# Kernel tuning notes

Hardware: AMD Instinct MI355X
Metric: run time of the kernel (lower is better)

## Reference

```python
import jax, jax.numpy as jnp
import numpy as np

B = 64          # batch of trees
L = 10          # gated internal levels below the root
H = 256         # hidden_size
E = 256         # embed_size
V = 64          # embedding vocab (relation/role types)
TOTAL = 2 ** (L + 1) - 2   # heap layout: level i (1..L) has 2^i nodes at offset 2^i - 2


def setup_inputs() -> dict:
    key = jax.random.key(0)
    k = jax.random.split(key, 7)
    s = 0.05
    return {
        "node_ids": jax.random.randint(k[0], (B, TOTAL), 0, V, dtype=jnp.int32),
        "emb_table": jax.random.normal(k[1], (V, E), jnp.float32) * s,
        # W: x-projections, order (forget, input, output, update)
        "W": jax.random.normal(k[2], (4, E, H), jnp.float32) * s,
        "bW": jax.random.normal(k[3], (4, H), jnp.float32) * s,
        # U: hidden projections, [gate, child] with gate order
        # (forget_left, forget_right, input, output, update), child order (left, right)
        "U": jax.random.normal(k[4], (5, 2, H, H), jnp.float32) * s,
        "Ws": jax.random.normal(k[5], (2 * H, 3), jnp.float32) * s,
        "bs": jax.random.normal(k[6], (3,), jnp.float32) * s,
    }


def _tree_lstm(node_ids, emb_table, W, bW, U, Ws, bs):
    Bn, total = node_ids.shape
    Lv = int(np.log2(total + 2)) - 1          # number of gated levels (static)
    Hh = U.shape[-1]
    # Wforget is shared by both forget gates (as in the original module)
    gate_map = jnp.array([0, 0, 1, 2, 3])      # x-projection index per gate
    h = c = None
    for lev in range(Lv, 0, -1):               # leaves-up level order
        n = 2 ** lev
        off = 2 ** lev - 2
        ids = node_ids[:, off:off + n]         # [B, n]
        x = emb_table[ids]                     # [B, n, E]
        xg = jnp.einsum('bne,geh->gbnh', x, W) + bW[:, None, None, :]  # [4,B,n,H]
        if h is None:
            # deepest level: children are leaves -> zero h and c (init_hidden())
            hl = hr = cl = cr = jnp.zeros((Bn, n, Hh), x.dtype)
        else:
            hl, hr = h[:, 0::2], h[:, 1::2]
            cl, cr = c[:, 0::2], c[:, 1::2]
        pre = (jnp.einsum('bnh,ghk->gbnk', hl, U[:, 0])
               + jnp.einsum('bnh,ghk->gbnk', hr, U[:, 1])
               + xg[gate_map])                 # [5,B,n,H]
        f_l = jax.nn.sigmoid(pre[0])
        f_r = jax.nn.sigmoid(pre[1])
        i_g = jax.nn.sigmoid(pre[2])
        o_g = jax.nn.sigmoid(pre[3])
        u_g = jnp.tanh(pre[4])
        c = i_g * u_g + f_l * cl + f_r * cr
        h = o_g * jnp.tanh(c)
    # root: concatenate the two children's hidden states, then score
    root_hidden = jnp.concatenate([h[:, 0], h[:, 1]], axis=-1)   # [B, 2H]
    scores = root_hidden @ Ws + bs                               # [B, 3]
    return scores, root_hidden


def reference(node_ids, emb_table, W, bW, U, Ws, bs):
    return _tree_lstm(node_ids, emb_table, W, bW, U, Ws, bs)
```

## Files before the change

### kernel.cpp

```cpp
#include <hip/hip_runtime.h>
#include <hip/hip_bf16.h>
#include <stdint.h>
#include <math.h>


typedef __bf16 bf16x8 __attribute__((ext_vector_type(8)));
typedef float  f32x4  __attribute__((ext_vector_type(4)));
typedef int    i32x4  __attribute__((ext_vector_type(4)));

__device__ __forceinline__ float sigf(float x) { return 1.f / (1.f + __expf(-x)); }
__device__ __forceinline__ float tanhfast(float x) {
    return 1.f - 2.f / (__expf(2.f * x) + 1.f);
}

__global__ void prep_kernel(const float* __restrict__ emb, const float* __restrict__ W,
                            const float* __restrict__ bW, const float* __restrict__ U,
                            float* __restrict__ xg4, __bf16* __restrict__ BtP) {
    if (blockIdx.x < 256) {
        int g = blockIdx.x >> 6, v = blockIdx.x & 63, k = threadIdx.x;
        __shared__ float e[256];
        e[k] = emb[v * 256 + k];
        __syncthreads();
        float s = bW[g * 256 + k];
        const float* Wg = W + g * 65536 + k;
#pragma unroll 4
        for (int i = 0; i < 256; i++) s += e[i] * Wg[i * 256];
        xg4[(v * 256 + k) * 4 + g] = s;
    } else {
        int t = (blockIdx.x - 256) * 256 + threadIdx.x;
        int g    = t >> 14;
        int r    = t & 16383;
        int ct   = r >> 10;
        int ks   = (r >> 6) & 15;
        int lane = t & 63;
        int lr = lane & 15, q = lane >> 4;
        int col = ct * 16 + lr;
        int kbase = ks * 32 + q * 8;
        bf16x8 v8;
#pragma unroll
        for (int e2 = 0; e2 < 8; e2++) {
            int k = kbase + e2;
            int s = k >> 8, kk = k & 255;
            v8[e2] = (__bf16)U[((g * 2 + s) * 256 + kk) * 256 + col];
        }
        *(bf16x8*)(BtP + (long)t * 8) = v8;
    }
}

__global__ void leaf_kernel(const int* __restrict__ ids, const float* __restrict__ xg4,
                            __bf16* __restrict__ h, __bf16* __restrict__ c) {
    int col = threadIdx.x;
    int r0 = blockIdx.x * 32;
    for (int r = r0; r < r0 + 32; r++) {
        int b = r >> 10, j = r & 1023;
        int id = ids[b * 2046 + 1022 + j];
        f32x4 xv = *(const f32x4*)(xg4 + (id * 256 + col) * 4);
        float ig = sigf(xv.y);
        float og = sigf(xv.z);
        float ug = tanhfast(xv.w);
        float cv = ig * ug;
        float hv = og * tanhfast(cv);
        h[r * 256 + col] = (__bf16)hv;
        c[r * 256 + col] = (__bf16)cv;
    }
}

__global__ __launch_bounds__(1024, 4) void level_kernel(
    const __bf16* __restrict__ A, const __bf16* __restrict__ Cprev,
    const __bf16* __restrict__ BtP, const float* __restrict__ xg4,
    const int* __restrict__ ids, __bf16* __restrict__ h_out,
    __bf16* __restrict__ c_out, float* __restrict__ rh_out,
    int lev, int M, int RG, int NB, int NB16) {
    __shared__ __bf16 Blds[5 * 16 * 512];
    const int gid = blockIdx.x;
    int rgslot, ct;
    if (NB16) { rgslot = gid & 15; ct = gid >> 4; }
    else      { rgslot = gid % NB; ct = gid / NB; }
    const int tid  = threadIdx.x;
    const int wave = tid >> 6;
    const int lane = tid & 63;
    const int lr = lane & 15, q = lane >> 4;
    const int gcol = ct * 16 + lr;
    const int n = 1 << lev;

#pragma unroll
    for (int i = 0; i < 5; i++) {
        int cc = tid + i * 1024;
        int g = cc >> 10;
        int r = cc & 1023;
        *(i32x4*)(&Blds[g * 8192 + r * 8]) =
            *(const i32x4*)(BtP + (long)(g * 16 + ct) * 8192 + r * 8);
    }
    __syncthreads();

    int rg0 = rgslot;
    long wrow = (long)rg0 * 512 + wave * 32;
    const __bf16* Ap = A + (wrow + lr) * 512 + q * 8;
    bf16x8 af[4][2];
    if (wrow < M) {
#pragma unroll
        for (int mt = 0; mt < 2; mt++) {
            af[0][mt] = *(const bf16x8*)(Ap + mt * 8192);
            af[1][mt] = *(const bf16x8*)(Ap + mt * 8192 + 32);
        }
    }

    for (int rg = rg0; rg < RG; rg += NB) {
        wrow = (long)rg * 512 + wave * 32;
        const bool active = (wrow < M);

        int rgn = rg + NB;
        long wrown = (rgn < RG) ? ((long)rgn * 512 + wave * 32) : wrow;
        const __bf16* Apn = A + (wrown + lr) * 512 + q * 8;

        int idv[2][4];
        __bf16 clv[2][4], crv[2][4];
        if (active) {
#pragma unroll
            for (int mt = 0; mt < 2; mt++)
#pragma unroll
                for (int v = 0; v < 4; v++) {
                    long grow = wrow + mt * 16 + q * 4 + v;
                    int b = (int)(grow >> lev);
                    int j = (int)(grow & (n - 1));
                    idv[mt][v] = ids[b * 2046 + (n - 2) + j];
                    clv[mt][v] = Cprev[grow * 512 + gcol];
                    crv[mt][v] = Cprev[grow * 512 + 256 + gcol];
                }
        }

        if (active) {
            f32x4 acc[5][2];
#pragma unroll
            for (int g2 = 0; g2 < 5; g2++)
#pragma unroll
                for (int mt = 0; mt < 2; mt++)
                    acc[g2][mt] = (f32x4){0.f, 0.f, 0.f, 0.f};

            bf16x8 bb[2][5];
#pragma unroll
            for (int g2 = 0; g2 < 5; g2++)
                bb[0][g2] = *(const bf16x8*)(&Blds[g2 * 8192 + lane * 8]);

#pragma unroll
            for (int s = 0; s < 16; s++) {
                {
                    int sp = s + 2;
                    const __bf16* P = (sp < 16) ? Ap : Apn;
                    int so = sp & 15;
#pragma unroll
                    for (int mt = 0; mt < 2; mt++)
                        af[sp & 3][mt] = *(const bf16x8*)(P + mt * 8192 + so * 32);
                }
                if (s + 1 < 16) {
#pragma unroll
                    for (int g2 = 0; g2 < 5; g2++)
                        bb[(s + 1) & 1][g2] =
                            *(const bf16x8*)(&Blds[g2 * 8192 + (s + 1) * 512 + lane * 8]);
                }
#pragma unroll
                for (int g2 = 0; g2 < 5; g2++)
#pragma unroll
                    for (int mt = 0; mt < 2; mt++)
                        acc[g2][mt] = __builtin_amdgcn_mfma_f32_16x16x32_bf16(
                            af[s & 3][mt], bb[s & 1][g2], acc[g2][mt], 0, 0, 0);
            }

#pragma unroll
            for (int mt = 0; mt < 2; mt++) {
#pragma unroll
                for (int v = 0; v < 4; v++) {
                    long grow = wrow + mt * 16 + q * 4 + v;
                    f32x4 xv = *(const f32x4*)(xg4 + (idv[mt][v] * 256 + gcol) * 4);
                    float fl = sigf(acc[0][mt][v] + xv.x);
                    float fr = sigf(acc[1][mt][v] + xv.x);
                    float ig = sigf(acc[2][mt][v] + xv.y);
                    float og = sigf(acc[3][mt][v] + xv.z);
                    float ug = tanhfast(acc[4][mt][v] + xv.w);
                    float cv = ig * ug + fl * (float)clv[mt][v]
                                       + fr * (float)crv[mt][v];
                    float hv = og * tanhfast(cv);
                    h_out[grow * 256 + gcol] = (__bf16)hv;
                    c_out[grow * 256 + gcol] = (__bf16)cv;
                    if (rh_out) rh_out[grow * 256 + gcol] = hv;
                }
            }
        }
        Ap = Apn;
    }
}

__global__ __launch_bounds__(1024, 4) void tail_kernel(
    const __bf16* __restrict__ Hin, const __bf16* __restrict__ Cin,
    const __bf16* __restrict__ BtP, const float* __restrict__ xg4,
    const int* __restrict__ ids, const float* __restrict__ Ws,
    const float* __restrict__ bs, float* __restrict__ out) {
    __shared__ __bf16 hbuf[96 * 256];
    __shared__ __bf16 cbuf[96 * 256];
    const int b    = blockIdx.x;
    const int tid  = threadIdx.x;
    const int wave = tid >> 6;
    const int lane = tid & 63;
    const int lr = lane & 15, q = lane >> 4;
    const int ct   = wave;
    const int gcol = ct * 16 + lr;

#pragma unroll
    for (int i = 0; i < 2; i++) {
        int idx = tid + i * 1024;
        int row = idx >> 5;
        int colb = (idx & 31) * 16;
        int dst = (row * 512 + colb) ^ (((row >> 1) & 7) << 4);
        *(i32x4*)((char*)hbuf + dst) =
            *(const i32x4*)(Hin + (long)(b * 64 + row) * 256 + (idx & 31) * 8);
        *(i32x4*)((char*)cbuf + dst) =
            *(const i32x4*)(Cin + (long)(b * 64 + row) * 256 + (idx & 31) * 8);
    }
    __syncthreads();

    const __bf16* Bbase = BtP + (long)ct * 8192 + lane * 8;

#pragma unroll 1
    for (int lev = 5; lev >= 1; lev--) {
        const int n   = 1 << lev;
        const int off = n - 2;
        const int p   = (5 - lev) & 1;
        const int rr  = p ? 64 : 0;
        const int wr  = p ? 0 : 64;
        const int mts = (n > 16) ? 2 : 1;

        int idv[2][4];
#pragma unroll
        for (int mt = 0; mt < 2; mt++)
#pragma unroll
            for (int v = 0; v < 4; v++) {
                int j = mt * 16 + q * 4 + v;
                idv[mt][v] = ids[b * 2046 + off + ((j < n) ? j : 0)];
            }

        f32x4 acc[5][2];
#pragma unroll
        for (int g2 = 0; g2 < 5; g2++)
#pragma unroll
            for (int mt = 0; mt < 2; mt++)
                acc[g2][mt] = (f32x4){0.f, 0.f, 0.f, 0.f};

        const __bf16* bp0 = Bbase;
        const __bf16* bp1 = Bbase + 131072;
        const __bf16* bp2 = Bbase + 262144;
        const __bf16* bp3 = Bbase + 393216;
        const __bf16* bp4 = Bbase + 524288;

#pragma unroll 1
        for (int s = 0; s < 16; s++) {
            bf16x8 bbv[5];
            bbv[0] = *(const bf16x8*)bp0;
            bbv[1] = *(const bf16x8*)bp1;
            bbv[2] = *(const bf16x8*)bp2;
            bbv[3] = *(const bf16x8*)bp3;
            bbv[4] = *(const bf16x8*)bp4;
            bp0 += 512; bp1 += 512; bp2 += 512; bp3 += 512; bp4 += 512;

            bf16x8 afv[2];
            {
                int k0 = q * 8 + s * 32;
                int crow = rr + 2 * lr + (k0 >> 8);
                int ab = (crow * 512 + (k0 & 255) * 2) ^ (((crow >> 1) & 7) << 4);
                afv[0] = *(const bf16x8*)((const char*)hbuf + ab);
            }
            if (mts > 1) {
                int k0 = q * 8 + s * 32;
                int crow = rr + 2 * (16 + lr) + (k0 >> 8);
                int ab = (crow * 512 + (k0 & 255) * 2) ^ (((crow >> 1) & 7) << 4);
                afv[1] = *(const bf16x8*)((const char*)hbuf + ab);
            } else {
                afv[1] = afv[0];
            }

#pragma unroll
            for (int g2 = 0; g2 < 5; g2++)
#pragma unroll
                for (int mt = 0; mt < 2; mt++)
                    acc[g2][mt] = __builtin_amdgcn_mfma_f32_16x16x32_bf16(
                        afv[mt], bbv[g2], acc[g2][mt], 0, 0, 0);
        }

#pragma unroll
        for (int mt = 0; mt < 2; mt++) {
#pragma unroll
            for (int v = 0; v < 4; v++) {
                int j = mt * 16 + q * 4 + v;
                if (mt < mts && j < n) {
                    int c0r = rr + 2 * j, c1r = rr + 2 * j + 1;
                    int a0 = (c0r * 512 + gcol * 2) ^ (((c0r >> 1) & 7) << 4);
                    int a1 = (c1r * 512 + gcol * 2) ^ (((c1r >> 1) & 7) << 4);
                    float cl = (float)*(const __bf16*)((const char*)cbuf + a0);
                    float cr = (float)*(const __bf16*)((const char*)cbuf + a1);
                    f32x4 xv = *(const f32x4*)(xg4 + (idv[mt][v] * 256 + gcol) * 4);
                    float fl = sigf(acc[0][mt][v] + xv.x);
                    float fr = sigf(acc[1][mt][v] + xv.x);
                    float ig = sigf(acc[2][mt][v] + xv.y);
                    float og = sigf(acc[3][mt][v] + xv.z);
                    float ug = tanhfast(acc[4][mt][v] + xv.w);
                    float cv = ig * ug + fl * cl + fr * cr;
                    float hv = og * tanhfast(cv);
                    int drow = wr + j;
                    int dst = (drow * 512 + gcol * 2) ^ (((drow >> 1) & 7) << 4);
                    *(__bf16*)((char*)hbuf + dst) = (__bf16)hv;
                    if (lev > 1) *(__bf16*)((char*)cbuf + dst) = (__bf16)cv;
                    if (lev == 1) out[192 + b * 512 + j * 256 + gcol] = hv;
                }
            }
        }
        __syncthreads();
    }

    if (tid < 192) {
        int t = tid >> 6, ln = tid & 63;
        float s = 0.f;
        for (int i = ln; i < 512; i += 64) {
            int row = 64 + (i >> 8);
            float hv = (float)hbuf[row * 256 + (i & 255)];
            s += hv * Ws[i * 3 + t];
        }
        for (int o = 32; o > 0; o >>= 1) s += __shfl_down(s, o);
        if (ln == 0) out[b * 3 + t] = s + bs[t];
    }
}

extern "C" void kernel_launch(void* const* d_in, const int* in_sizes, int n_in,
                              void* d_out, int out_size, void* d_ws, size_t ws_size,
                              hipStream_t stream) {
    const int*   ids = (const int*)  d_in[0];
    const float* emb = (const float*)d_in[1];
    const float* W   = (const float*)d_in[2];
    const float* bW  = (const float*)d_in[3];
    const float* U   = (const float*)d_in[4];
    const float* Ws  = (const float*)d_in[5];
    const float* bs  = (const float*)d_in[6];
    float* out = (float*)d_out;

    char* ws = (char*)d_ws;
    float*  xg4 = (float*)ws;
    __bf16* BtP = (__bf16*)(ws + 262144);
    __bf16* h0  = (__bf16*)(ws + 1572864);
    __bf16* c0  = (__bf16*)(ws + 35127296);
    __bf16* h1  = (__bf16*)(ws + 68681728);
    __bf16* c1  = (__bf16*)(ws + 85458944);

    prep_kernel<<<dim3(576), dim3(256), 0, stream>>>(emb, W, bW, U, xg4, BtP);
    leaf_kernel<<<dim3(2048), dim3(256), 0, stream>>>(ids, xg4, h0, c0);

    __bf16* hb[2] = {h0, h1};
    __bf16* cb[2] = {c0, c1};
    int cur = 0;
    for (int lev = 9; lev >= 6; lev--) {
        int M = 64 << lev;
        int RG = M >> 9;
        int NB = (RG < 16) ? RG : 16;
        level_kernel<<<dim3(16 * NB), dim3(1024), 0, stream>>>(
            hb[cur], cb[cur], BtP, xg4, ids, hb[1 - cur], cb[1 - cur], nullptr,
            lev, M, RG, NB, (NB == 16) ? 1 : 0);
        cur = 1 - cur;
    }
    tail_kernel<<<dim3(64), dim3(1024), 0, stream>>>(
        hb[cur], cb[cur], BtP, xg4, ids, Ws, bs, out);
}
```

Measured before the change: 369.1 us.

## Fuse tree level 6 into the per-tree tail kernel

Level 6 is now computed inside the tail kernel, which loads 128 child rows per tree into LDS and processes them in two chunks of 32 parents using MFMA, writing results back into LDS. This removes one level_kernel launch and its global h/c write and read. In exchange, level-6 work is spread over only 64 blocks instead of a wider grid, and LDS use per block grows to 128KB.

```diff
diff --git a/kernel.cpp b/kernel.cpp
--- a/kernel.cpp
+++ b/kernel.cpp
@@ -195,8 +195,8 @@
     const __bf16* __restrict__ BtP, const float* __restrict__ xg4,
     const int* __restrict__ ids, const float* __restrict__ Ws,
     const float* __restrict__ bs, float* __restrict__ out) {
-    __shared__ __bf16 hbuf[96 * 256];
-    __shared__ __bf16 cbuf[96 * 256];
+    __shared__ __bf16 hbuf[128 * 256];
+    __shared__ __bf16 cbuf[128 * 256];
     const int b    = blockIdx.x;
     const int tid  = threadIdx.x;
     const int wave = tid >> 6;
@@ -206,19 +206,111 @@
     const int gcol = ct * 16 + lr;
 
 #pragma unroll
-    for (int i = 0; i < 2; i++) {
+    for (int i = 0; i < 4; i++) {
         int idx = tid + i * 1024;
         int row = idx >> 5;
         int colb = (idx & 31) * 16;
         int dst = (row * 512 + colb) ^ (((row >> 1) & 7) << 4);
         *(i32x4*)((char*)hbuf + dst) =
-            *(const i32x4*)(Hin + (long)(b * 64 + row) * 256 + (idx & 31) * 8);
+            *(const i32x4*)(Hin + (long)(b * 128 + row) * 256 + (idx & 31) * 8);
         *(i32x4*)((char*)cbuf + dst) =
-            *(const i32x4*)(Cin + (long)(b * 64 + row) * 256 + (idx & 31) * 8);
+            *(const i32x4*)(Cin + (long)(b * 128 + row) * 256 + (idx & 31) * 8);
     }
     __syncthreads();
 
     const __bf16* Bbase = BtP + (long)ct * 8192 + lane * 8;
+
+#pragma unroll 1
+    for (int ch = 0; ch < 2; ch++) {
+        const int rbase = ch * 32;
+
+        int idv6[2][4];
+        float clv6[2][4], crv6[2][4];
+#pragma unroll
+        for (int mt = 0; mt < 2; mt++)
+#pragma unroll
+            for (int v = 0; v < 4; v++) {
+                int j = rbase + mt * 16 + q * 4 + v;
+                idv6[mt][v] = ids[b * 2046 + 62 + j];
+                int c0r = 2 * j, c1r = 2 * j + 1;
+                int a0 = (c0r * 512 + gcol * 2) ^ (((c0r >> 1) & 7) << 4);
+                int a1 = (c1r * 512 + gcol * 2) ^ (((c1r >> 1) & 7) << 4);
+                clv6[mt][v] = (float)*(const __bf16*)((const char*)cbuf + a0);
+                crv6[mt][v] = (float)*(const __bf16*)((const char*)cbuf + a1);
+            }
+
+        f32x4 acc[5][2];
+#pragma unroll
+        for (int g2 = 0; g2 < 5; g2++)
+#pragma unroll
+            for (int mt = 0; mt < 2; mt++)
+                acc[g2][mt] = (f32x4){0.f, 0.f, 0.f, 0.f};
+
+        const __bf16* bp0 = Bbase;
+        const __bf16* bp1 = Bbase + 131072;
+        const __bf16* bp2 = Bbase + 262144;
+        const __bf16* bp3 = Bbase + 393216;
+        const __bf16* bp4 = Bbase + 524288;
+
+#pragma unroll 1
+        for (int s = 0; s < 16; s++) {
+            bf16x8 bbv[5];
+            bbv[0] = *(const bf16x8*)bp0;
+            bbv[1] = *(const bf16x8*)bp1;
+            bbv[2] = *(const bf16x8*)bp2;
+            bbv[3] = *(const bf16x8*)bp3;
+            bbv[4] = *(const bf16x8*)bp4;
+            bp0 += 512; bp1 += 512; bp2 += 512; bp3 += 512; bp4 += 512;
+
+            bf16x8 afv[2];
+            int k0 = q * 8 + s * 32;
+            {
+                int crow = 2 * (rbase + lr) + (k0 >> 8);
+                int ab = (crow * 512 + (k0 & 255) * 2) ^ (((crow >> 1) & 7) << 4);
+                afv[0] = *(const bf16x8*)((const char*)hbuf + ab);
+            }
+            {
+                int crow = 2 * (rbase + 16 + lr) + (k0 >> 8);
+                int ab = (crow * 512 + (k0 & 255) * 2) ^ (((crow >> 1) & 7) << 4);
+                afv[1] = *(const bf16x8*)((const char*)hbuf + ab);
+            }
+
+#pragma unroll
+            for (int g2 = 0; g2 < 5; g2++)
+#pragma unroll
+                for (int mt = 0; mt < 2; mt++)
+                    acc[g2][mt] = __builtin_amdgcn_mfma_f32_16x16x32_bf16(
+                        afv[mt], bbv[g2], acc[g2][mt], 0, 0, 0);
+        }
+
+        float hv6[2][4], cv6[2][4];
+#pragma unroll
+        for (int mt = 0; mt < 2; mt++)
+#pragma unroll
+            for (int v = 0; v < 4; v++) {
+                f32x4 xv = *(const f32x4*)(xg4 + (idv6[mt][v] * 256 + gcol) * 4);
+                float fl = sigf(acc[0][mt][v] + xv.x);
+                float fr = sigf(acc[1][mt][v] + xv.x);
+                float ig = sigf(acc[2][mt][v] + xv.y);
+                float og = sigf(acc[3][mt][v] + xv.z);
+                float ug = tanhfast(acc[4][mt][v] + xv.w);
+                float cv = ig * ug + fl * clv6[mt][v] + fr * crv6[mt][v];
+                cv6[mt][v] = cv;
+                hv6[mt][v] = og * tanhfast(cv);
+            }
+        __syncthreads();
+
+#pragma unroll
+        for (int mt = 0; mt < 2; mt++)
+#pragma unroll
+            for (int v = 0; v < 4; v++) {
+                int j = rbase + mt * 16 + q * 4 + v;
+                int dst = (j * 512 + gcol * 2) ^ (((j >> 1) & 7) << 4);
+                *(__bf16*)((char*)hbuf + dst) = (__bf16)hv6[mt][v];
+                *(__bf16*)((char*)cbuf + dst) = (__bf16)cv6[mt][v];
+            }
+        __syncthreads();
+    }
 
 #pragma unroll 1
     for (int lev = 5; lev >= 1; lev--) {
@@ -354,7 +446,7 @@
     __bf16* hb[2] = {h0, h1};
     __bf16* cb[2] = {c0, c1};
     int cur = 0;
-    for (int lev = 9; lev >= 6; lev--) {
+    for (int lev = 9; lev >= 7; lev--) {
         int M = 64 << lev;
         int RG = M >> 9;
         int NB = (RG < 16) ? RG : 16;
```

Result: no change. 375.6 us (+1.8%).
